# Optimization experiments

Hardware: AMD Instinct MI355X
Metric: run time of the kernel (lower is better)

Reference implementation:

```python
import jax, jax.numpy as jnp
import numpy as np

B, S, D, H, DH, L, MLP, VOCAB = 1, 2048, 512, 8, 64, 6, 2048, 256
BLOCK, C = 128, 32
EPS = 1e-6
NEG = -1e9


def layer_norm(x, scale, bias):
    mu = jnp.mean(x, axis=-1, keepdims=True)
    var = jnp.mean(jnp.square(x - mu), axis=-1, keepdims=True)
    return (x - mu) * jax.lax.rsqrt(var + EPS) * scale + bias


def sparse_pattern_mask(seq_len):
    # Union of Fixed1 (same causal block) and Fixed2 (last c columns of each
    # block), both intersected with the causal mask. Shape [S, S] bool.
    i = jnp.arange(seq_len)[:, None]
    j = jnp.arange(seq_len)[None, :]
    causal = j <= i
    fixed1 = (i // BLOCK) == (j // BLOCK)
    fixed2 = (j % BLOCK) >= (BLOCK - C)
    return causal & (fixed1 | fixed2)


def setup_inputs() -> dict:
    key = jax.random.key(0)
    ks = jax.random.split(key, 12)
    s = 0.02
    inp = {
        'tokens': jax.random.randint(ks[0], (B, S), 0, VOCAB, dtype=jnp.int32),
        'embed': jax.random.normal(ks[1], (VOCAB, D), jnp.float32) * s,
        'pos_emb': jax.random.normal(ks[2], (1, S, D), jnp.float32) * s,
        'ln1_scale': jnp.ones((L, D), jnp.float32),
        'ln1_bias': jnp.zeros((L, D), jnp.float32),
        'wq': jax.random.normal(ks[3], (L, D, H, DH), jnp.float32) * s,
        'wk': jax.random.normal(ks[4], (L, D, H, DH), jnp.float32) * s,
        'wv': jax.random.normal(ks[5], (L, D, H, DH), jnp.float32) * s,
        'wo': jax.random.normal(ks[6], (L, H, DH, D), jnp.float32) * s,
        'ln2_scale': jnp.ones((L, D), jnp.float32),
        'ln2_bias': jnp.zeros((L, D), jnp.float32),
        'w1': jax.random.normal(ks[7], (L, D, MLP), jnp.float32) * s,
        'b1': jnp.zeros((L, MLP), jnp.float32),
        'w2': jax.random.normal(ks[8], (L, MLP, D), jnp.float32) * s,
        'b2': jnp.zeros((L, D), jnp.float32),
        'lnf_scale': jnp.ones((D,), jnp.float32),
        'lnf_bias': jnp.zeros((D,), jnp.float32),
        'wout': jax.random.normal(ks[9], (D, VOCAB), jnp.float32) * s,
        'bout': jnp.zeros((VOCAB,), jnp.float32),
    }
    return inp


def _forward(tokens, embed, pos_emb, ln1_scale, ln1_bias, wq, wk, wv, wo,
             ln2_scale, ln2_bias, w1, b1, w2, b2, lnf_scale, lnf_bias,
             wout, bout):
    # padding mask computed on unshifted inputs (keys with token==0 are masked)
    key_pad = tokens > 0                               # [B, S]
    # shift right (decoder teacher forcing)
    shifted = jnp.pad(tokens, ((0, 0), (1, 0)))[:, :-1]
    x = embed[shifted] + pos_emb                       # [B, S, D]

    pattern = sparse_pattern_mask(S)                   # [S, S]
    mask = pattern[None, None] & key_pad[:, None, None, :]  # [B,1,S,S]

    for l in range(L):
        h = layer_norm(x, ln1_scale[l], ln1_bias[l])
        q = jnp.einsum('bsd,dhk->bshk', h, wq[l]) / jnp.sqrt(
            jnp.asarray(DH, x.dtype))
        k = jnp.einsum('bsd,dhk->bshk', h, wk[l])
        v = jnp.einsum('bsd,dhk->bshk', h, wv[l])
        scores = jnp.einsum('bqhk,bshk->bhqs', q, k)   # [B,H,S,S]
        scores = jnp.where(mask, scores, NEG)
        probs = jax.nn.softmax(scores, axis=-1)
        o = jnp.einsum('bhqs,bshk->bqhk', probs, v)
        x = x + jnp.einsum('bqhk,hkd->bqd', o, wo[l])

        y = layer_norm(x, ln2_scale[l], ln2_bias[l])
        y = jax.nn.gelu(y @ w1[l] + b1[l])
        x = x + (y @ w2[l] + b2[l])

    x = layer_norm(x, lnf_scale, lnf_bias)
    return x @ wout + bout                             # [B, S, VOCAB]


def reference(tokens, embed, pos_emb, ln1_scale, ln1_bias, wq, wk, wv, wo,
              ln2_scale, ln2_bias, w1, b1, w2, b2, lnf_scale, lnf_bias,
              wout, bout):
    return _forward(tokens, embed, pos_emb, ln1_scale, ln1_bias, wq, wk, wv,
                    wo, ln2_scale, ln2_bias, w1, b1, w2, b2, lnf_scale,
                    lnf_bias, wout, bout)
```

## Files before the change

### kernel.cpp

```cpp
#include <hip/hip_runtime.h>
#include <hip/hip_bf16.h>
#include <cstdint>
#include <cstddef>

#define DEV __device__ __forceinline__

namespace {

constexpr int S    = 2048;
constexpr int D    = 512;
constexpr int H    = 8;
constexpr int DH   = 64;
constexpr int NL   = 6;
constexpr int MLPD = 2048;
constexpr int VOC  = 256;
constexpr int QS   = 1536;
constexpr float EPSF = 1e-6f;

typedef unsigned short u16;
typedef __attribute__((ext_vector_type(8))) short s8v;
typedef __attribute__((ext_vector_type(4))) float f4v;

DEV float u2f(u16 u){
  union { unsigned int i; float f; } t; t.i = ((unsigned int)u) << 16; return t.f;
}
DEV short bfr(float f){
  __hip_bfloat16 h = __float2bfloat16(f);
  short s; __builtin_memcpy(&s, &h, 2); return s;
}
DEV float gelu_fast(float x){
  float z = 0.7978845608028654f * (x + 0.044715f * x * x * x);
  return x / (1.f + __expf(-2.f * z));
}

__global__ void k_embed(const int* __restrict__ tokens, const float* __restrict__ emb,
                        const float* __restrict__ pos, float* __restrict__ x){
  int s = blockIdx.x;
  int tok = (s == 0) ? 0 : tokens[s - 1];
  if (tok < 0) tok = 0; if (tok >= VOC) tok = VOC - 1;
  const float* er = emb + (size_t)tok * D;
  const float* pr = pos + (size_t)s * D;
  float* xr = x + (size_t)s * D;
  for (int d = threadIdx.x; d < D; d += blockDim.x)
    xr[d] = er[d] + pr[d];
}

template<int HASP>
__global__ __launch_bounds__(256)
void k_lnr(const float* __restrict__ P0, const float* __restrict__ P1,
           const float* __restrict__ bias, float* __restrict__ x,
           const float* __restrict__ sc, const float* __restrict__ bi,
           u16* __restrict__ out)
{
  int s = blockIdx.x * 4 + (threadIdx.x >> 6), t = threadIdx.x & 63;
  size_t base = (size_t)s * D;
  float v[8]; float sum = 0.f, sq = 0.f;
  #pragma unroll
  for (int e = 0; e < 8; ++e){
    int d = t + 64 * e;
    size_t idx = base + d;
    float xv = x[idx];
    if (HASP){
      float bv = bias ? bias[d] : 0.f;
      xv += P0[idx] + P1[idx] + bv;
      x[idx] = xv;
    }
    v[e] = xv; sum += xv; sq += xv * xv;
  }
  #pragma unroll
  for (int off = 32; off >= 1; off >>= 1){
    sum += __shfl_down(sum, off, 64);
    sq  += __shfl_down(sq,  off, 64);
  }
  sum = __shfl(sum, 0, 64); sq = __shfl(sq, 0, 64);
  float mu  = sum * (1.f / (float)D);
  float var = sq * (1.f / (float)D) - mu * mu;
  float r = rsqrtf(var + EPSF);
  u16* orow = out + base;
  #pragma unroll
  for (int e = 0; e < 8; ++e){
    int d = t + 64 * e;
    orow[d] = (u16)bfr((v[e] - mu) * r * sc[d] + bi[d]);
  }
}

__global__ __launch_bounds__(256)
void k_wt(const float* __restrict__ src, u16* __restrict__ dst, int R, int C,
          size_t sStr, size_t dStr){
  src += (size_t)blockIdx.z * sStr;
  dst += (size_t)blockIdx.z * dStr;
  __shared__ float tb[32][33];
  int c0 = blockIdx.x * 32, r0 = blockIdx.y * 32;
  int tc = threadIdx.x & 31, tr8 = threadIdx.x >> 5;
  #pragma unroll
  for (int rr = 0; rr < 32; rr += 8)
    tb[rr + tr8][tc] = src[(size_t)(r0 + rr + tr8) * C + c0 + tc];
  __syncthreads();
  #pragma unroll
  for (int rr = 0; rr < 32; rr += 8)
    dst[(size_t)(c0 + rr + tr8) * R + r0 + tc] = (u16)bfr(tb[tc][rr + tr8]);
}

__global__ __launch_bounds__(256)
void k_wt4(const float* __restrict__ wq, const float* __restrict__ wk,
           const float* __restrict__ wv, const float* __restrict__ wo,
           u16* __restrict__ wqkvT, u16* __restrict__ woT)
{
  const size_t L512 = (size_t)512 * 512;
  int fam = blockIdx.z / 6, l = blockIdx.z % 6;
  const float* src;
  u16* dst;
  if (fam == 0){ src = wq + (size_t)l * L512; dst = wqkvT + (size_t)l * QS * 512; }
  else if (fam == 1){ src = wk + (size_t)l * L512; dst = wqkvT + (size_t)l * QS * 512 + 512 * 512; }
  else if (fam == 2){ src = wv + (size_t)l * L512; dst = wqkvT + (size_t)l * QS * 512 + 1024 * 512; }
  else { src = wo + (size_t)l * L512; dst = woT + (size_t)l * L512; }
  __shared__ float tb[32][33];
  int c0 = blockIdx.x * 32, r0 = blockIdx.y * 32;
  int tc = threadIdx.x & 31, tr8 = threadIdx.x >> 5;
  #pragma unroll
  for (int rr = 0; rr < 32; rr += 8)
    tb[rr + tr8][tc] = src[(size_t)(r0 + rr + tr8) * 512 + c0 + tc];
  __syncthreads();
  #pragma unroll
  for (int rr = 0; rr < 32; rr += 8)
    dst[(size_t)(c0 + rr + tr8) * 512 + r0 + tc] = (u16)bfr(tb[tc][rr + tr8]);
}

template<int FM, int FN, int MODE>
__global__ __launch_bounds__(64)
void k_gd(const u16* __restrict__ A, const u16* __restrict__ Bt,
          const float* __restrict__ bias, float* __restrict__ Cf,
          u16* __restrict__ Cb, int N, int K, float alpha)
{
  const int nx = gridDim.x;
  const int nwg = nx * gridDim.y;
  int wg = blockIdx.y * nx + blockIdx.x;
  wg = (wg & 7) * (nwg >> 3) + (wg >> 3);
  const int m0 = (wg / nx) * (FM * 16), n0 = (wg % nx) * (FN * 16);
  const int lane = threadIdx.x, lr = lane & 15, lg = lane >> 4;
  const u16* ap = A  + (size_t)(m0 + lr) * K + lg * 8;
  const u16* bp = Bt + (size_t)(n0 + lr) * K + lg * 8;
  f4v acc[FM][FN] = {};
  #pragma unroll 4
  for (int k0 = 0; k0 < K; k0 += 32){
    s8v af[FM], bf[FN];
    #pragma unroll
    for (int fi = 0; fi < FM; ++fi)
      af[fi] = *reinterpret_cast<const s8v*>(ap + (size_t)fi * 16 * K + k0);
    #pragma unroll
    for (int fj = 0; fj < FN; ++fj)
      bf[fj] = *reinterpret_cast<const s8v*>(bp + (size_t)fj * 16 * K + k0);
    #pragma unroll
    for (int fi = 0; fi < FM; ++fi)
      #pragma unroll
      for (int fj = 0; fj < FN; ++fj)
        acc[fi][fj] = __builtin_amdgcn_mfma_f32_16x16x32_bf16(af[fi], bf[fj], acc[fi][fj], 0, 0, 0);
  }
  #pragma unroll
  for (int fi = 0; fi < FM; ++fi)
    #pragma unroll
    for (int fj = 0; fj < FN; ++fj)
      #pragma unroll
      for (int r = 0; r < 4; ++r){
        int row = m0 + fi * 16 + lg * 4 + r;
        int col = n0 + fj * 16 + lr;
        size_t idx = (size_t)row * N + col;
        float v = acc[fi][fj][r];
        if (MODE == 1)      Cb[idx] = (u16)bfr(gelu_fast(v + bias[col]));
        else if (MODE == 2) Cf[idx] += v + (bias ? bias[col] : 0.f);
        else if (MODE == 3) Cf[idx] = v + bias[col];
        else {
          float al = (col < 512) ? alpha : 1.f;
          Cb[idx] = (u16)bfr(v * al);
        }
      }
}

template<int MODE>
__global__ __launch_bounds__(256)
void k_gi(const u16* __restrict__ A, const u16* __restrict__ Bt,
          const float* __restrict__ bias, u16* __restrict__ vt,
          u16* __restrict__ Cb, int N, int K, float alpha)
{
  __shared__ float Ls[2][64][65];
  const int nx = gridDim.x;
  const int nwg = nx * gridDim.y;
  int wg = blockIdx.y * nx + blockIdx.x;
  wg = (wg & 7) * (nwg >> 3) + (wg >> 3);
  const int m0 = (wg / nx) * 64, n0 = (wg % nx) * 64;
  const int w = threadIdx.x >> 6, lane = threadIdx.x & 63;
  const int lr = lane & 15, lg = lane >> 4;
  const int KC = K >> 2;
  const u16* ap = A  + (size_t)(m0 + lr) * K + w * KC + lg * 8;
  const u16* bp = Bt + (size_t)(n0 + lr) * K + w * KC + lg * 8;
  f4v acc[4][4] = {};
  #pragma unroll 4
  for (int k0 = 0; k0 < KC; k0 += 32){
    s8v af[4], bf[4];
    #pragma unroll
    for (int fi = 0; fi < 4; ++fi)
      af[fi] = *reinterpret_cast<const s8v*>(ap + (size_t)fi * 16 * K + k0);
    #pragma unroll
    for (int fj = 0; fj < 4; ++fj)
      bf[fj] = *reinterpret_cast<const s8v*>(bp + (size_t)fj * 16 * K + k0);
    #pragma unroll
    for (int fi = 0; fi < 4; ++fi)
      #pragma unroll
      for (int fj = 0; fj < 4; ++fj)
        acc[fi][fj] = __builtin_amdgcn_mfma_f32_16x16x32_bf16(af[fi], bf[fj], acc[fi][fj], 0, 0, 0);
  }
  if (w >= 2){
    #pragma unroll
    for (int fi = 0; fi < 4; ++fi)
      #pragma unroll
      for (int fj = 0; fj < 4; ++fj)
        #pragma unroll
        for (int r = 0; r < 4; ++r)
          Ls[w - 2][lane][fi * 16 + fj * 4 + r] = acc[fi][fj][r];
  }
  __syncthreads();
  if (w < 2){
    #pragma unroll
    for (int fi = 0; fi < 4; ++fi)
      #pragma unroll
      for (int fj = 0; fj < 4; ++fj)
        #pragma unroll
        for (int r = 0; r < 4; ++r)
          acc[fi][fj][r] += Ls[w][lane][fi * 16 + fj * 4 + r];
    if (w == 1){
      #pragma unroll
      for (int fi = 0; fi < 4; ++fi)
        #pragma unroll
        for (int fj = 0; fj < 4; ++fj)
          #pragma unroll
          for (int r = 0; r < 4; ++r)
            Ls[1][lane][fi * 16 + fj * 4 + r] = acc[fi][fj][r];
    }
  }
  __syncthreads();
  if (w == 0){
    #pragma unroll
    for (int fi = 0; fi < 4; ++fi)
      #pragma unroll
      for (int fj = 0; fj < 4; ++fj)
        #pragma unroll
        for (int r = 0; r < 4; ++r){
          acc[fi][fj][r] += Ls[1][lane][fi * 16 + fj * 4 + r];
          Ls[0][lane][fi * 16 + fj * 4 + r] = acc[fi][fj][r];
        }
  }
  __syncthreads();
  #pragma unroll
  for (int fj = 0; fj < 4; ++fj)
    #pragma unroll
    for (int r = 0; r < 4; ++r){
      float v = Ls[0][lane][w * 16 + fj * 4 + r];
      int row = m0 + w * 16 + lg * 4 + r;
      int col = n0 + fj * 16 + lr;
      if (MODE == 1){
        Cb[(size_t)row * N + col] = (u16)bfr(gelu_fast(v + bias[col]));
      } else {
        if (col < 512){
          Cb[(size_t)row * N + col] = (u16)bfr(v * alpha);
        } else if (col < 1024){
          Cb[(size_t)row * N + col] = (u16)bfr(v);
        } else {
          vt[(size_t)(col - 1024) * S + row] = (u16)bfr(v);
        }
      }
    }
}

template<int FM, int FN>
__global__ __launch_bounds__(64)
void k_gds(const u16* __restrict__ A, const u16* __restrict__ Bt,
           float* __restrict__ P, int N, int K, int KC)
{
  const int nx = gridDim.x;
  const int nwg = nx * gridDim.y;
  const int M = gridDim.y * (FM * 16);
  int wg = blockIdx.y * nx + blockIdx.x;
  wg = (wg & 7) * (nwg >> 3) + (wg >> 3);
  const int m0 = (wg / nx) * (FM * 16), n0 = (wg % nx) * (FN * 16);
  const int z = blockIdx.z;
  const int lane = threadIdx.x, lr = lane & 15, lg = lane >> 4;
  const u16* ap = A  + (size_t)(m0 + lr) * K + z * KC + lg * 8;
  const u16* bp = Bt + (size_t)(n0 + lr) * K + z * KC + lg * 8;
  P += (size_t)z * M * N;
  f4v acc[FM][FN] = {};
  #pragma unroll 4
  for (int k0 = 0; k0 < KC; k0 += 32){
    s8v af[FM], bf[FN];
    #pragma unroll
    for (int fi = 0; fi < FM; ++fi)
      af[fi] = *reinterpret_cast<const s8v*>(ap + (size_t)fi * 16 * K + k0);
    #pragma unroll
    for (int fj = 0; fj < FN; ++fj)
      bf[fj] = *reinterpret_cast<const s8v*>(bp + (size_t)fj * 16 * K + k0);
    #pragma unroll
    for (int fi = 0; fi < FM; ++fi)
      #pragma unroll
      for (int fj = 0; fj < FN; ++fj)
        acc[fi][fj] = __builtin_amdgcn_mfma_f32_16x16x32_bf16(af[fi], bf[fj], acc[fi][fj], 0, 0, 0);
  }
  #pragma unroll
  for (int fi = 0; fi < FM; ++fi)
    #pragma unroll
    for (int fj = 0; fj < FN; ++fj)
      #pragma unroll
      for (int r = 0; r < 4; ++r){
        int row = m0 + fi * 16 + lg * 4 + r;
        int col = n0 + fj * 16 + lr;
        P[(size_t)row * N + col] = acc[fi][fj][r];
      }
}

__global__ __launch_bounds__(64)
void k_mattn(const u16* __restrict__ qp_, const u16* __restrict__ kp_,
             const u16* __restrict__ vt, const int* __restrict__ tokens,
             u16* __restrict__ ob)
{
  const int q0 = (gridDim.x - 1 - blockIdx.x) * 16;
  const int h  = blockIdx.y;
  const int B  = q0 >> 7;
  const int lane = threadIdx.x, lr = lane & 15, lg = lane >> 4;

  __shared__ __align__(16) u16 Ps[16][40];

  const u16* qrow = qp_ + (size_t)(q0 + lr) * QS + h * DH;
  s8v qf0 = *reinterpret_cast<const s8v*>(qrow + lg * 8);
  s8v qf1 = *reinterpret_cast<const s8v*>(qrow + 32 + lg * 8);

  f4v o0 = {}, o1 = {}, o2 = {}, o3 = {};
  float m[4] = {-1e30f, -1e30f, -1e30f, -1e30f};
  float l[4] = {0.f, 0.f, 0.f, 0.f};

  const int ntiles = B + ((q0 & 127) >> 5) + 1;

  for (int tt = 0; tt < ntiles; ++tt){
    int kbase; bool causal;
    if (tt < B){ kbase = tt * 128 + 96; causal = false; }
    else       { kbase = B * 128 + (tt - B) * 32; causal = (kbase + 31 > q0); }

    f4v s0 = {}, s1 = {};
    const u16* k0p = kp_ + (size_t)(kbase + lr) * QS + h * DH;
    const u16* k1p = kp_ + (size_t)(kbase + 16 + lr) * QS + h * DH;
    s8v kf;
    kf = *reinterpret_cast<const s8v*>(k0p + lg * 8);
    s0 = __builtin_amdgcn_mfma_f32_16x16x32_bf16(qf0, kf, s0, 0, 0, 0);
    kf = *reinterpret_cast<const s8v*>(k0p + 32 + lg * 8);
    s0 = __builtin_amdgcn_mfma_f32_16x16x32_bf16(qf1, kf, s0, 0, 0, 0);
    kf = *reinterpret_cast<const s8v*>(k1p + lg * 8);
    s1 = __builtin_amdgcn_mfma_f32_16x16x32_bf16(qf0, kf, s1, 0, 0, 0);
    kf = *reinterpret_cast<const s8v*>(k1p + 32 + lg * 8);
    s1 = __builtin_amdgcn_mfma_f32_16x16x32_bf16(qf1, kf, s1, 0, 0, 0);

    const int tok0 = tokens[kbase + lr] > 0;
    const int tok1 = tokens[kbase + 16 + lr] > 0;
    #pragma unroll
    for (int r = 0; r < 4; ++r){
      int qg = q0 + 4 * lg + r;
      float a0 = (tok0 && (!causal || kbase + lr <= qg))      ? s0[r] : -1e30f;
      float a1 = (tok1 && (!causal || kbase + 16 + lr <= qg)) ? s1[r] : -1e30f;
      float tm = fmaxf(a0, a1);
      tm = fmaxf(tm, __shfl_xor(tm, 1, 64));
      tm = fmaxf(tm, __shfl_xor(tm, 2, 64));
      tm = fmaxf(tm, __shfl_xor(tm, 4, 64));
      tm = fmaxf(tm, __shfl_xor(tm, 8, 64));
      float mn = fmaxf(m[r], tm);
      bool dead = (mn <= -1e29f);
      float sc = dead ? 1.f : __expf(m[r] - mn);
      float p0 = dead ? 0.f : __expf(a0 - mn);
      float p1 = dead ? 0.f : __expf(a1 - mn);
      l[r] = l[r] * sc + p0 + p1;
      m[r] = mn;
      o0[r] *= sc; o1[r] *= sc; o2[r] *= sc; o3[r] *= sc;
      Ps[4 * lg + r][lr]      = (u16)bfr(p0);
      Ps[4 * lg + r][16 + lr] = (u16)bfr(p1);
    }

    asm volatile("s_waitcnt lgkmcnt(0)" ::: "memory");
    __builtin_amdgcn_sched_barrier(0);
    s8v pf  = *reinterpret_cast<const s8v*>(&Ps[lr][lg * 8]);
    const u16* vtb = vt + (size_t)(h * DH + lr) * S + kbase + lg * 8;
    s8v vf0 = *reinterpret_cast<const s8v*>(vtb);
    s8v vf1 = *reinterpret_cast<const s8v*>(vtb + (size_t)16 * S);
    s8v vf2 = *reinterpret_cast<const s8v*>(vtb + (size_t)32 * S);
    s8v vf3 = *reinterpret_cast<const s8v*>(vtb + (size_t)48 * S);
    o0 = __builtin_amdgcn_mfma_f32_16x16x32_bf16(pf, vf0, o0, 0, 0, 0);
    o1 = __builtin_amdgcn_mfma_f32_16x16x32_bf16(pf, vf1, o1, 0, 0, 0);
    o2 = __builtin_amdgcn_mfma_f32_16x16x32_bf16(pf, vf2, o2, 0, 0, 0);
    o3 = __builtin_amdgcn_mfma_f32_16x16x32_bf16(pf, vf3, o3, 0, 0, 0);
  }

  #pragma unroll
  for (int r = 0; r < 4; ++r){
    float lt = l[r];
    lt += __shfl_xor(lt, 1, 64);
    lt += __shfl_xor(lt, 2, 64);
    lt += __shfl_xor(lt, 4, 64);
    lt += __shfl_xor(lt, 8, 64);
    int qg = q0 + 4 * lg + r;
    u16* orow = ob + (size_t)qg * D + h * DH;
    if (lt <= 0.f){
      #pragma unroll
      for (int c4 = 0; c4 < 4; ++c4){
        const u16* vr = vt + (size_t)(h * DH + c4 * 16 + lr) * S;
        float s = 0.f;
        for (int j = 0; j < S; ++j) s += u2f(vr[j]);
        orow[c4 * 16 + lr] = (u16)bfr(s * (1.f / (float)S));
      }
    } else {
      float inv = 1.f / lt;
      orow[lr]      = (u16)bfr(o0[r] * inv);
      orow[16 + lr] = (u16)bfr(o1[r] * inv);
      orow[32 + lr] = (u16)bfr(o2[r] * inv);
      orow[48 + lr] = (u16)bfr(o3[r] * inv);
    }
  }
}

}

extern "C" void kernel_launch(void* const* d_in, const int* in_sizes, int n_in,
                              void* d_out, int out_size, void* d_ws, size_t ws_size,
                              hipStream_t stream)
{
  (void)n_in; (void)out_size; (void)ws_size;

  int I_tok=0, I_emb=1, I_pos=2, I_l1s=3, I_l1b=4, I_wq=5, I_wk=6, I_wv=7,
      I_wo=8, I_l2s=9, I_l2b=10, I_w1=11, I_b1=12, I_w2=13, I_b2=14,
      I_lfs=15, I_lfb=16, I_wout=17, I_bout=18;
  if (in_sizes[0] != S){
    I_b1=0;  I_b2=1;  I_bout=2; I_emb=3;  I_l1b=4; I_l1s=5;  I_l2b=6;
    I_l2s=7; I_lfb=8; I_lfs=9;  I_pos=10; I_tok=11; I_w1=12; I_w2=13;
    I_wk=14; I_wo=15; I_wout=16; I_wq=17; I_wv=18;
  }

  const int*   tokens = (const int*)d_in[I_tok];
  const float* emb  = (const float*)d_in[I_emb];
  const float* pos  = (const float*)d_in[I_pos];
  const float* ln1s = (const float*)d_in[I_l1s];
  const float* ln1b = (const float*)d_in[I_l1b];
  const float* wq   = (const float*)d_in[I_wq];
  const float* wk   = (const float*)d_in[I_wk];
  const float* wv   = (const float*)d_in[I_wv];
  const float* wo   = (const float*)d_in[I_wo];
  const float* ln2s = (const float*)d_in[I_l2s];
  const float* ln2b = (const float*)d_in[I_l2b];
  const float* w1   = (const float*)d_in[I_w1];
  const float* b1   = (const float*)d_in[I_b1];
  const float* w2   = (const float*)d_in[I_w2];
  const float* b2   = (const float*)d_in[I_b2];
  const float* lnfs = (const float*)d_in[I_lfs];
  const float* lnfb = (const float*)d_in[I_lfb];
  const float* wout = (const float*)d_in[I_wout];
  const float* bout = (const float*)d_in[I_bout];
  float* outp = (float*)d_out;

  char* ws = (char*)d_ws;
  float* x    = (float*)(ws);
  u16*  hb    = (u16*)(ws + ((size_t)4  << 20));
  u16*  qkvb  = (u16*)(ws + ((size_t)6  << 20));
  u16*  ob    = (u16*)(ws + ((size_t)12 << 20));
  u16*  gb    = (u16*)(ws + ((size_t)14 << 20));
  u16*  vtb   = (u16*)(ws + ((size_t)14 << 20));
  float* pWO  = (float*)(ws + ((size_t)14 << 20));
  float* pW2  = (float*)(ws + ((size_t)6  << 20));
  u16*  wqkvT = (u16*)(ws + ((size_t)23 << 20));
  u16*  w1T   = (u16*)(ws + ((size_t)32 << 20));
  u16*  w2T   = (u16*)(ws + ((size_t)44 << 20));
  u16*  woT   = (u16*)(ws + ((size_t)56 << 20));
  u16*  woutT = (u16*)(ws + ((size_t)59 << 20));

  const size_t L512 = (size_t)512 * 512;
  const size_t LMLP = (size_t)512 * 2048;
  const size_t SM   = (size_t)S * 512;

  k_wt4<<<dim3(16, 16, 24), dim3(256), 0, stream>>>(wq, wk, wv, wo, wqkvT, woT);
  k_wt<<<dim3(64, 16, 6), dim3(256), 0, stream>>>(w1, w1T, 512, 2048, LMLP, LMLP);
  k_wt<<<dim3(16, 64, 6), dim3(256), 0, stream>>>(w2, w2T, 2048, 512, LMLP, LMLP);
  k_wt<<<dim3(8,  16, 1), dim3(256), 0, stream>>>(wout, woutT, 512, 256, 0, 0);

  k_embed<<<dim3(S), dim3(128), 0, stream>>>(tokens, emb, pos, x);

  for (int l = 0; l < NL; ++l){
    if (l == 0){
      k_lnr<0><<<dim3(S/4), dim3(256), 0, stream>>>(
          nullptr, nullptr, nullptr, x, ln1s, ln1b, hb);
    }
    k_gi<4><<<dim3(24, 32), dim3(256), 0, stream>>>(
        hb, wqkvT + (size_t)l * QS * 512, nullptr, vtb, qkvb, QS, 512, 0.125f);
    k_mattn<<<dim3(S/16, H), dim3(64), 0, stream>>>(
        qkvb, qkvb + 512, vtb, tokens, ob);
    k_gds<2,4><<<dim3(8, 64, 2), dim3(64), 0, stream>>>(
        ob, woT + (size_t)l * L512, pWO, 512, 512, 256);
    k_lnr<1><<<dim3(S/4), dim3(256), 0, stream>>>(
        pWO, pWO + SM, nullptr, x, ln2s + (size_t)l*D, ln2b + (size_t)l*D, hb);
    k_gi<1><<<dim3(32, 32), dim3(256), 0, stream>>>(
        hb, w1T + (size_t)l * LMLP, b1 + (size_t)l*MLPD, nullptr, gb, MLPD, 512, 1.f);
    k_gds<2,4><<<dim3(8, 64, 2), dim3(64), 0, stream>>>(
        gb, w2T + (size_t)l * LMLP, pW2, 512, 2048, 1024);
    if (l < NL - 1){
      k_lnr<1><<<dim3(S/4), dim3(256), 0, stream>>>(
          pW2, pW2 + SM, b2 + (size_t)l*D, x,
          ln1s + (size_t)(l+1)*D, ln1b + (size_t)(l+1)*D, hb);
    } else {
      k_lnr<1><<<dim3(S/4), dim3(256), 0, stream>>>(
          pW2, pW2 + SM, b2 + (size_t)l*D, x, lnfs, lnfb, hb);
    }
  }

  k_gd<2,4,3><<<dim3(4, 64), dim3(64), 0, stream>>>(
      hb, woutT, bout, outp, nullptr, VOC, 512, 1.f);
}
```

Measured before the change: 756.6 us.

## Use 128x128 LDS-tiled GEMM with direct global-to-LDS loads for MLP up-projection

Result: faster. 735.5 us (-2.8%).

```diff
diff --git a/kernel.cpp b/kernel.cpp
--- a/kernel.cpp
+++ b/kernel.cpp
@@ -31,6 +31,11 @@
 DEV float gelu_fast(float x){
   float z = 0.7978845608028654f * (x + 0.044715f * x * x * x);
   return x / (1.f + __expf(-2.f * z));
+}
+DEV void gll16(const u16* gp, u16* lp){
+  __builtin_amdgcn_global_load_lds(
+      (const __attribute__((address_space(1))) unsigned int*)gp,
+      (__attribute__((address_space(3))) unsigned int*)lp, 16, 0, 0);
 }
 
 __global__ void k_embed(const int* __restrict__ tokens, const float* __restrict__ emb,
@@ -173,6 +178,61 @@
           float al = (col < 512) ? alpha : 1.f;
           Cb[idx] = (u16)bfr(v * al);
         }
+      }
+}
+
+template<int MODE>
+__global__ __launch_bounds__(256)
+void k_gs(const u16* __restrict__ A, const u16* __restrict__ Bt,
+          const float* __restrict__ bias, u16* __restrict__ Cb,
+          int N, int K)
+{
+  __shared__ __align__(16) u16 As[128 * 32];
+  __shared__ __align__(16) u16 Bs[128 * 32];
+  const int nx = gridDim.x;
+  const int nwg = nx * gridDim.y;
+  int wg = blockIdx.y * nx + blockIdx.x;
+  wg = (wg & 7) * (nwg >> 3) + (wg >> 3);
+  const int m0 = (wg / nx) * 128, n0 = (wg % nx) * 128;
+  const int w = threadIdx.x >> 6, lane = threadIdx.x & 63;
+  const int lr = lane & 15, lg = lane >> 4;
+  const int wr = w >> 1, wc = w & 1;
+  const int srow = lane >> 2, schk = lane & 3;
+  f4v acc[4][4] = {};
+  for (int k0 = 0; k0 < K; k0 += 32){
+    __syncthreads();
+    #pragma unroll
+    for (int i = 0; i < 2; ++i){
+      int j = w * 2 + i;
+      int row = j * 16 + srow;
+      gll16(A  + (size_t)(m0 + row) * K + k0 + schk * 8, As + j * 512);
+      gll16(Bt + (size_t)(n0 + row) * K + k0 + schk * 8, Bs + j * 512);
+    }
+    asm volatile("s_waitcnt vmcnt(0)" ::: "memory");
+    __syncthreads();
+    s8v af[4], bf[4];
+    #pragma unroll
+    for (int fi = 0; fi < 4; ++fi)
+      af[fi] = *reinterpret_cast<const s8v*>(As + (wr * 64 + fi * 16 + lr) * 32 + lg * 8);
+    #pragma unroll
+    for (int fj = 0; fj < 4; ++fj)
+      bf[fj] = *reinterpret_cast<const s8v*>(Bs + (wc * 64 + fj * 16 + lr) * 32 + lg * 8);
+    #pragma unroll
+    for (int fi = 0; fi < 4; ++fi)
+      #pragma unroll
+      for (int fj = 0; fj < 4; ++fj)
+        acc[fi][fj] = __builtin_amdgcn_mfma_f32_16x16x32_bf16(af[fi], bf[fj], acc[fi][fj], 0, 0, 0);
+  }
+  #pragma unroll
+  for (int fi = 0; fi < 4; ++fi)
+    #pragma unroll
+    for (int fj = 0; fj < 4; ++fj)
+      #pragma unroll
+      for (int r = 0; r < 4; ++r){
+        int row = m0 + wr * 64 + fi * 16 + lg * 4 + r;
+        int col = n0 + wc * 64 + fj * 16 + lr;
+        float v = acc[fi][fj][r];
+        if (MODE == 1) Cb[(size_t)row * N + col] = (u16)bfr(gelu_fast(v + bias[col]));
       }
 }
 
@@ -497,8 +557,8 @@
         ob, woT + (size_t)l * L512, pWO, 512, 512, 256);
     k_lnr<1><<<dim3(S/4), dim3(256), 0, stream>>>(
         pWO, pWO + SM, nullptr, x, ln2s + (size_t)l*D, ln2b + (size_t)l*D, hb);
-    k_gi<1><<<dim3(32, 32), dim3(256), 0, stream>>>(
-        hb, w1T + (size_t)l * LMLP, b1 + (size_t)l*MLPD, nullptr, gb, MLPD, 512, 1.f);
+    k_gs<1><<<dim3(16, 16), dim3(256), 0, stream>>>(
+        hb, w1T + (size_t)l * LMLP, b1 + (size_t)l*MLPD, gb, MLPD, 512);
     k_gds<2,4><<<dim3(8, 64, 2), dim3(64), 0, stream>>>(
         gb, w2T + (size_t)l * LMLP, pW2, 512, 2048, 1024);
     if (l < NL - 1){
```
